# Optimization experiments

Hardware: AMD Instinct MI355X
Metric: run time of the kernel (lower is better)

## Reference

```python
import jax, jax.numpy as jnp
import numpy as np

N_EMBD = 64
N_HEAD = 8
HEAD_SIZE = N_EMBD // N_HEAD  # 8
BLOCK_SIZE = 64
B = 4096
SCALE = N_EMBD ** (-0.5)  # NOTE: source scales by C**-0.5 with C=n_embd, not head_size
EPS = 1e-5


def setup_inputs() -> dict:
    key = jax.random.key(0)
    ks = jax.random.split(key, 12)
    s = 0.02
    return {
        "x": jax.random.normal(ks[0], (B, BLOCK_SIZE, N_EMBD), jnp.float32),
        # per-head q/k/v projections packed as [C, H, hs] (no bias in source)
        "Wq": jax.random.normal(ks[1], (N_EMBD, N_HEAD, HEAD_SIZE), jnp.float32) * s,
        "Wk": jax.random.normal(ks[2], (N_EMBD, N_HEAD, HEAD_SIZE), jnp.float32) * s,
        "Wv": jax.random.normal(ks[3], (N_EMBD, N_HEAD, HEAD_SIZE), jnp.float32) * s,
        "Wo": jax.random.normal(ks[4], (N_EMBD, N_EMBD), jnp.float32) * s,
        "bo": jnp.zeros((N_EMBD,), jnp.float32),
        "W1": jax.random.normal(ks[5], (N_EMBD, 4 * N_EMBD), jnp.float32) * s,
        "b1": jnp.zeros((4 * N_EMBD,), jnp.float32),
        "W2": jax.random.normal(ks[6], (4 * N_EMBD, N_EMBD), jnp.float32) * s,
        "b2": jnp.zeros((N_EMBD,), jnp.float32),
        "g1": jnp.ones((N_EMBD,), jnp.float32),
        "be1": jnp.zeros((N_EMBD,), jnp.float32),
        "g2": jnp.ones((N_EMBD,), jnp.float32),
        "be2": jnp.zeros((N_EMBD,), jnp.float32),
    }


def _layernorm(x, g, b):
    mu = jnp.mean(x, axis=-1, keepdims=True)
    var = jnp.mean(jnp.square(x - mu), axis=-1, keepdims=True)
    return (x - mu) * jax.lax.rsqrt(var + EPS) * g + b


def reference(x, Wq, Wk, Wv, Wo, bo, W1, b1, W2, b2, g1, be1, g2, be2):
    Bb, T, C = x.shape
    # --- multi-head causal self-attention (dropout = identity in eval) ---
    h = _layernorm(x, g1, be1)
    q = jnp.einsum('btc,chd->bhtd', h, Wq)
    k = jnp.einsum('btc,chd->bhtd', h, Wk)
    v = jnp.einsum('btc,chd->bhtd', h, Wv)
    wei = jnp.einsum('bhtd,bhsd->bhts', q, k) * SCALE
    mask = jnp.tril(jnp.ones((T, T), dtype=bool))
    wei = jnp.where(mask, wei, -jnp.inf)
    wei = jax.nn.softmax(wei, axis=-1)
    attn = jnp.einsum('bhts,bhsd->bhtd', wei, v)
    attn = attn.transpose(0, 2, 1, 3).reshape(Bb, T, C)  # concat heads
    x = x + attn @ Wo + bo
    # --- feed-forward ---
    h2 = _layernorm(x, g2, be2)
    ff = jax.nn.relu(h2 @ W1 + b1) @ W2 + b2
    return x + ff
```

## Files before the change

kernel.cpp:

```cpp
#include <hip/hip_runtime.h>
#include <hip/hip_bf16.h>


typedef __attribute__((ext_vector_type(8))) short short8;
typedef __attribute__((ext_vector_type(4))) float f32x4;

#if __has_builtin(__builtin_amdgcn_exp2f)
#define EXP2F(x) __builtin_amdgcn_exp2f(x)
#else
#define EXP2F(x) __expf((x) * 0.69314718056f)
#endif
#if __has_builtin(__builtin_amdgcn_rcpf)
#define RCPF(x) __builtin_amdgcn_rcpf(x)
#else
#define RCPF(x) (1.0f / (x))
#endif

#define ST  72
#define STU 136
#define OH  0
#define OKK 4608
#define OV  9216
#define OP  13896
#define OU  4608
#define NSH 18504

__device__ __forceinline__ short f2bf(float f) {
    unsigned int u = __float_as_uint(f);
    u += 0x7fffu + ((u >> 16) & 1u);
    return (short)(u >> 16);
}
__device__ __forceinline__ unsigned pk2(float a, float b) {
    float2 t; t.x = a; t.y = b;
    __hip_bfloat162 h = __float22bfloat162_rn(t);
    unsigned u; __builtin_memcpy(&u, &h, 4); return u;
}
__device__ __forceinline__ f32x4 mfma16(short8 a, short8 b, f32x4 c) {
    return __builtin_amdgcn_mfma_f32_16x16x32_bf16(a, b, c, 0, 0, 0);
}

__global__ __launch_bounds__(64) void prepack_kernel(
    const float* __restrict__ Wq, const float* __restrict__ Wk,
    const float* __restrict__ Wv, const float* __restrict__ Wo,
    const float* __restrict__ W1, const float* __restrict__ W2,
    short* __restrict__ ws)
{
    int gid = blockIdx.x * 64 + threadIdx.x;
    int lane = gid & 63;
    int fid  = gid >> 6;
    int quad = lane >> 4, nn = lane & 15;
    short8 o;
    if (fid < 24) {
        int tile = fid >> 1, ks = fid & 1;
        const float* Ws = (tile < 4) ? Wq : ((tile < 8) ? Wk : Wv);
        float scale = (tile < 4) ? 0.18033688011f : 1.0f;
        int col = (tile & 3) * 16 + nn;
#pragma unroll
        for (int j = 0; j < 8; ++j)
            o[j] = f2bf(Ws[(ks * 32 + quad * 8 + j) * 64 + col] * scale);
    } else if (fid < 32) {
        int idx = fid - 24, nt = idx >> 1, ks = idx & 1;
#pragma unroll
        for (int j = 0; j < 8; ++j)
            o[j] = f2bf(Wo[(ks * 32 + quad * 8 + j) * 64 + nt * 16 + nn]);
    } else if (fid < 64) {
        int idx = fid - 32, c = idx >> 3, tile = (idx >> 1) & 3, ks = idx & 1;
#pragma unroll
        for (int j = 0; j < 8; ++j)
            o[j] = f2bf(W1[(ks * 32 + quad * 8 + j) * 256 + c * 64 + tile * 16 + nn]);
    } else {
        int idx = fid - 64, c = idx >> 3, nt = (idx >> 1) & 3, ks = idx & 1;
#pragma unroll
        for (int j = 0; j < 8; ++j)
            o[j] = f2bf(W2[(c * 64 + ks * 32 + quad * 8 + j) * 64 + nt * 16 + nn]);
    }
    *(short8*)(ws + (size_t)gid * 8) = o;
}

__global__ __launch_bounds__(256, 4) void block_kernel(
    const float* __restrict__ x,
    const float* __restrict__ bo,
    const float* __restrict__ b1,
    const float* __restrict__ b2,
    const float* __restrict__ g1, const float* __restrict__ be1,
    const float* __restrict__ g2, const float* __restrict__ be2,
    const short8* __restrict__ WB,
    float* __restrict__ out)
{
    __shared__ short sm[NSH];
    const int tid  = threadIdx.x;
    const int wv   = tid >> 6;
    const int lane = tid & 63;
    const int quad = lane >> 4;
    const int nn   = lane & 15;
    const int t_my = wv * 16 + nn;
    const int b    = blockIdx.x;
    const float* xb = x + (size_t)b * 4096;
    const f32x4 zf = {0.f, 0.f, 0.f, 0.f};
    const short8 z8 = {0, 0, 0, 0, 0, 0, 0, 0};

    if (tid < ST) sm[OV + 64 * ST + tid] = (short)0x3F80;
    float xr[16];
    float gv[4], bv[4];
#pragma unroll
    for (int nt = 0; nt < 4; ++nt) { gv[nt] = g1[nt * 16 + nn]; bv[nt] = be1[nt * 16 + nn]; }
#pragma unroll
    for (int nt = 0; nt < 4; ++nt)
#pragma unroll
        for (int r = 0; r < 4; ++r)
            xr[nt * 4 + r] = xb[(wv * 16 + quad * 4 + r) * 64 + nt * 16 + nn];
#pragma unroll
    for (int r = 0; r < 4; ++r) {
        float s1 = 0.f, s2 = 0.f;
#pragma unroll
        for (int nt = 0; nt < 4; ++nt) { float v = xr[nt * 4 + r]; s1 += v; s2 += v * v; }
        s1 += __shfl_xor(s1, 1); s1 += __shfl_xor(s1, 2); s1 += __shfl_xor(s1, 4); s1 += __shfl_xor(s1, 8);
        s2 += __shfl_xor(s2, 1); s2 += __shfl_xor(s2, 2); s2 += __shfl_xor(s2, 4); s2 += __shfl_xor(s2, 8);
        float mu = s1 * 0.015625f;
        float rstd = rsqrtf(s2 * 0.015625f - mu * mu + 1e-5f);
        int base = OH + (wv * 16 + quad * 4 + r) * ST + nn;
#pragma unroll
        for (int nt = 0; nt < 4; ++nt)
            sm[base + nt * 16] = f2bf((xr[nt * 4 + r] - mu) * rstd * gv[nt] + bv[nt]);
    }

    unsigned qp[8];
    {
        short8 hf0 = *(const short8*)&sm[OH + t_my * ST + quad * 8];
        short8 hf1 = *(const short8*)&sm[OH + t_my * ST + 32 + quad * 8];
#pragma unroll
        for (int jt = 0; jt < 4; ++jt) {
            f32x4 a = mfma16(WB[(size_t)(jt * 2 + 0) * 64 + lane], hf0, zf);
            a = mfma16(WB[(size_t)(jt * 2 + 1) * 64 + lane], hf1, a);
            qp[jt * 2 + 0] = pk2(a[0], a[1]);
            qp[jt * 2 + 1] = pk2(a[2], a[3]);
        }
#pragma unroll
        for (int jt = 0; jt < 4; ++jt) {
            f32x4 a = mfma16(WB[(size_t)((4 + jt) * 2 + 0) * 64 + lane], hf0, zf);
            a = mfma16(WB[(size_t)((4 + jt) * 2 + 1) * 64 + lane], hf1, a);
            uint2 w; w.x = pk2(a[0], a[1]); w.y = pk2(a[2], a[3]);
            *(uint2*)&sm[OKK + t_my * ST + jt * 16 + quad * 4] = w;
        }
#pragma unroll
        for (int dt = 0; dt < 4; ++dt) {
            f32x4 a = mfma16(hf0, WB[(size_t)((8 + dt) * 2 + 0) * 64 + lane], zf);
            a = mfma16(hf1, WB[(size_t)((8 + dt) * 2 + 1) * 64 + lane], a);
            uint2 w; w.x = pk2(a[0], a[1]); w.y = pk2(a[2], a[3]);
            *(uint2*)&sm[OV + (dt * 16 + nn) * ST + wv * 16 + quad * 4] = w;
        }
    }
    __syncthreads();

    const bool keep0 = (quad * 4 + 0) <= nn, keep1 = (quad * 4 + 1) <= nn;
    const bool keep2 = (quad * 4 + 2) <= nn, keep3 = (quad * 4 + 3) <= nn;
    const int arow_base = (nn < 8) ? nn : 64;
    const int arow_step = (nn < 8) ? 8 : 0;
    const int nks = (wv < 2) ? 1 : 2;
    const int zhi = nks * 2;
#pragma unroll 1
    for (int h = 0; h < 8; ++h) {
        short8 bq;
        {
            int qsA = ((h & 1) * 2) * 16 + nn, qsB = qsA + 16;
            int qi = (h >> 1) * 2;
            union { unsigned u[4]; short8 s; } bb;
            bb.u[0] = __shfl(qp[qi + 0], qsA);
            bb.u[1] = __shfl(qp[qi + 1], qsA);
            bb.u[2] = __shfl(qp[qi + 0], qsB);
            bb.u[3] = __shfl(qp[qi + 1], qsB);
            bq = bb.s;
        }
        for (int mt = 0; mt <= wv; ++mt) {
            short8 ak = z8;
            if (quad == 0) ak = *(const short8*)&sm[OKK + (mt * 16 + nn) * ST + h * 8];
            f32x4 s = mfma16(ak, bq, zf);
            float e0 = EXP2F(s[0]), e1 = EXP2F(s[1]), e2 = EXP2F(s[2]), e3 = EXP2F(s[3]);
            if (mt == wv) {
                e0 = keep0 ? e0 : 0.f; e1 = keep1 ? e1 : 0.f;
                e2 = keep2 ? e2 : 0.f; e3 = keep3 ? e3 : 0.f;
            }
            uint2 w; w.x = pk2(e0, e1); w.y = pk2(e2, e3);
            *(uint2*)&sm[OP + t_my * ST + mt * 16 + quad * 4] = w;
        }
        for (int mt = wv + 1; mt < zhi; ++mt) {
            uint2 w; w.x = 0u; w.y = 0u;
            *(uint2*)&sm[OP + t_my * ST + mt * 16 + quad * 4] = w;
        }
        const int arow = arow_base + h * arow_step;
        f32x4 pv = zf;
        for (int ks = 0; ks < nks; ++ks) {
            short8 av = *(const short8*)&sm[OV + arow * ST + ks * 32 + quad * 8];
            short8 bp = *(const short8*)&sm[OP + t_my * ST + ks * 32 + quad * 8];
            pv = mfma16(av, bp, pv);
        }
        float denom = __shfl(pv[0], 32 + nn);
        float rd = RCPF(denom);
        if (quad < 2) {
            uint2 w; w.x = pk2(pv[0] * rd, pv[1] * rd); w.y = pk2(pv[2] * rd, pv[3] * rd);
            *(uint2*)&sm[OH + t_my * ST + h * 8 + quad * 4] = w;
        }
    }

    {
        short8 aa0 = *(const short8*)&sm[OH + t_my * ST + quad * 8];
        short8 aa1 = *(const short8*)&sm[OH + t_my * ST + 32 + quad * 8];
#pragma unroll
        for (int nt = 0; nt < 4; ++nt) {
            f32x4 oa = mfma16(aa0, WB[(size_t)(24 + nt * 2 + 0) * 64 + lane], zf);
            oa = mfma16(aa1, WB[(size_t)(24 + nt * 2 + 1) * 64 + lane], oa);
            float bov = bo[nt * 16 + nn];
#pragma unroll
            for (int r = 0; r < 4; ++r) xr[nt * 4 + r] += oa[r] + bov;
        }
    }
#pragma unroll
    for (int nt = 0; nt < 4; ++nt) { gv[nt] = g2[nt * 16 + nn]; bv[nt] = be2[nt * 16 + nn]; }
#pragma unroll
    for (int r = 0; r < 4; ++r) {
        float s1 = 0.f, s2 = 0.f;
#pragma unroll
        for (int nt = 0; nt < 4; ++nt) { float v = xr[nt * 4 + r]; s1 += v; s2 += v * v; }
        s1 += __shfl_xor(s1, 1); s1 += __shfl_xor(s1, 2); s1 += __shfl_xor(s1, 4); s1 += __shfl_xor(s1, 8);
        s2 += __shfl_xor(s2, 1); s2 += __shfl_xor(s2, 2); s2 += __shfl_xor(s2, 4); s2 += __shfl_xor(s2, 8);
        float mu = s1 * 0.015625f;
        float rstd = rsqrtf(s2 * 0.015625f - mu * mu + 1e-5f);
        int base = OP + (wv * 16 + quad * 4 + r) * ST + nn;
#pragma unroll
        for (int nt = 0; nt < 4; ++nt)
            sm[base + nt * 16] = f2bf((xr[nt * 4 + r] - mu) * rstd * gv[nt] + bv[nt]);
    }
    short8 h2f0 = *(const short8*)&sm[OP + t_my * ST + quad * 8];
    short8 h2f1 = *(const short8*)&sm[OP + t_my * ST + 32 + quad * 8];
    __syncthreads();

    f32x4 fa[4];
#pragma unroll
    for (int nt = 0; nt < 4; ++nt) fa[nt] = zf;
#pragma unroll
    for (int c = 0; c < 2; ++c) {
#pragma unroll
        for (int tile = 0; tile < 8; ++tile) {
            int gc = c * 8 + tile;
            int fid = 32 + (gc >> 2) * 8 + (gc & 3) * 2;
            f32x4 u = mfma16(WB[(size_t)fid * 64 + lane], h2f0, zf);
            u = mfma16(WB[(size_t)(fid + 1) * 64 + lane], h2f1, u);
            const float4 bb = *(const float4*)&b1[gc * 16 + quad * 4];
            float u0 = fmaxf(u[0] + bb.x, 0.f), u1 = fmaxf(u[1] + bb.y, 0.f);
            float u2 = fmaxf(u[2] + bb.z, 0.f), u3 = fmaxf(u[3] + bb.w, 0.f);
            uint2 w; w.x = pk2(u0, u1); w.y = pk2(u2, u3);
            *(uint2*)&sm[OU + t_my * STU + tile * 16 + quad * 4] = w;
        }
#pragma unroll
        for (int ks = 0; ks < 4; ++ks) {
            short8 au = *(const short8*)&sm[OU + t_my * STU + ks * 32 + quad * 8];
            int gk = c * 4 + ks;
            int fidb = 64 + (gk >> 1) * 8 + (gk & 1);
#pragma unroll
            for (int nt = 0; nt < 4; ++nt)
                fa[nt] = mfma16(au, WB[(size_t)(fidb + nt * 2) * 64 + lane], fa[nt]);
        }
    }

    float* ob = out + (size_t)b * 4096;
#pragma unroll
    for (int nt = 0; nt < 4; ++nt) {
        float b2v = b2[nt * 16 + nn];
#pragma unroll
        for (int r = 0; r < 4; ++r)
            ob[(wv * 16 + quad * 4 + r) * 64 + nt * 16 + nn] = xr[nt * 4 + r] + fa[nt][r] + b2v;
    }
}

extern "C" void kernel_launch(void* const* d_in, const int* in_sizes, int n_in,
                              void* d_out, int out_size, void* d_ws, size_t ws_size,
                              hipStream_t stream) {
    const float* x   = (const float*)d_in[0];
    const float* Wq  = (const float*)d_in[1];
    const float* Wk  = (const float*)d_in[2];
    const float* Wv  = (const float*)d_in[3];
    const float* Wo  = (const float*)d_in[4];
    const float* bo  = (const float*)d_in[5];
    const float* W1  = (const float*)d_in[6];
    const float* b1  = (const float*)d_in[7];
    const float* W2  = (const float*)d_in[8];
    const float* b2  = (const float*)d_in[9];
    const float* g1  = (const float*)d_in[10];
    const float* be1 = (const float*)d_in[11];
    const float* g2  = (const float*)d_in[12];
    const float* be2 = (const float*)d_in[13];
    short* ws = (short*)d_ws;
    prepack_kernel<<<dim3(96), dim3(64), 0, stream>>>(Wq, Wk, Wv, Wo, W1, W2, ws);
    const int nb = in_sizes[0] / 4096;
    block_kernel<<<dim3(nb), dim3(256), 0, stream>>>(
        x, bo, b1, b2, g1, be1, g2, be2, (const short8*)ws, (float*)d_out);
}
```

Measured before the change: 203.1 us.

## Keep softmax probabilities in registers via shuffles, drop P buffer, raise occupancy

The exponentiated attention scores no longer go through a shared-memory P buffer. They stay in registers and are redistributed into the PV MFMA operand layout with wave shuffles. Dropping the P region shrinks shared memory, and launch bounds go from 4 to 5 blocks per CU. The second layernorm output now reuses the H region. The LN conversions use packed bf16 conversion. The changes trade LDS traffic for many more shuffles and higher register pressure under the tighter occupancy bound.

Measured after the change: 214.7 us. 5.7% more time.

```diff
diff --git a/kernel.cpp b/kernel.cpp
--- a/kernel.cpp
+++ b/kernel.cpp
@@ -21,9 +21,8 @@
 #define OH  0
 #define OKK 4608
 #define OV  9216
-#define OP  13896
 #define OU  4608
-#define NSH 18504
+#define NSH 13896
 
 __device__ __forceinline__ short f2bf(float f) {
     unsigned int u = __float_as_uint(f);
@@ -77,7 +76,36 @@
     *(short8*)(ws + (size_t)gid * 8) = o;
 }
 
-__global__ __launch_bounds__(256, 4) void block_kernel(
+#define QK_TILE(mt, WX, WY)                                                   \
+    {                                                                         \
+        short8 ak = z8;                                                       \
+        if (quad == 0) ak = *(const short8*)&sm[OKK + ((mt) * 16 + nn) * ST + h * 8]; \
+        f32x4 s = mfma16(ak, bq, zf);                                         \
+        float e0 = EXP2F(s[0]), e1 = EXP2F(s[1]);                             \
+        float e2 = EXP2F(s[2]), e3 = EXP2F(s[3]);                             \
+        if ((mt) == wv) {                                                     \
+            e0 = keep0 ? e0 : 0.f; e1 = keep1 ? e1 : 0.f;                     \
+            e2 = keep2 ? e2 : 0.f; e3 = keep3 ? e3 : 0.f;                     \
+        }                                                                     \
+        WX = pk2(e0, e1); WY = pk2(e2, e3);                                   \
+    }
+
+#define PV_KS(ks, WXA, WYA, WXB, WYB)                                         \
+    {                                                                         \
+        unsigned a0 = __shfl(WXA, qa), a1 = __shfl(WXB, qa);                  \
+        unsigned b0 = __shfl(WYA, qa), b1 = __shfl(WYB, qa);                  \
+        unsigned c0 = __shfl(WXA, qb), c1 = __shfl(WXB, qb);                  \
+        unsigned d0 = __shfl(WYA, qb), d1 = __shfl(WYB, qb);                  \
+        union { unsigned u[4]; short8 s; } bb;                                \
+        bb.u[0] = loQ ? a0 : a1;                                              \
+        bb.u[1] = loQ ? b0 : b1;                                              \
+        bb.u[2] = loQ ? c0 : c1;                                              \
+        bb.u[3] = loQ ? d0 : d1;                                              \
+        short8 av = *(const short8*)&sm[OV + arow * ST + (ks) * 32 + quad * 8]; \
+        pv = mfma16(av, bb.s, pv);                                            \
+    }
+
+__global__ __launch_bounds__(256, 5) void block_kernel(
     const float* __restrict__ x,
     const float* __restrict__ bo,
     const float* __restrict__ b1,
@@ -119,9 +147,15 @@
         float mu = s1 * 0.015625f;
         float rstd = rsqrtf(s2 * 0.015625f - mu * mu + 1e-5f);
         int base = OH + (wv * 16 + quad * 4 + r) * ST + nn;
-#pragma unroll
-        for (int nt = 0; nt < 4; ++nt)
-            sm[base + nt * 16] = f2bf((xr[nt * 4 + r] - mu) * rstd * gv[nt] + bv[nt]);
+        float h0 = (xr[0 + r]  - mu) * rstd * gv[0] + bv[0];
+        float h1 = (xr[4 + r]  - mu) * rstd * gv[1] + bv[1];
+        float h2 = (xr[8 + r]  - mu) * rstd * gv[2] + bv[2];
+        float h3 = (xr[12 + r] - mu) * rstd * gv[3] + bv[3];
+        unsigned pA = pk2(h0, h1), pB = pk2(h2, h3);
+        sm[base +  0] = (short)pA;
+        sm[base + 16] = (short)(pA >> 16);
+        sm[base + 32] = (short)pB;
+        sm[base + 48] = (short)(pB >> 16);
     }
 
     unsigned qp[8];
@@ -157,7 +191,9 @@
     const int arow_base = (nn < 8) ? nn : 64;
     const int arow_step = (nn < 8) ? 8 : 0;
     const int nks = (wv < 2) ? 1 : 2;
-    const int zhi = nks * 2;
+    const int qa = (( 2 * quad)      & 3) * 16 + nn;
+    const int qb = ((2 * quad + 1) & 3) * 16 + nn;
+    const bool loQ = (quad < 2);
 #pragma unroll 1
     for (int h = 0; h < 8; ++h) {
         short8 bq;
@@ -171,29 +207,16 @@
             bb.u[3] = __shfl(qp[qi + 1], qsB);
             bq = bb.s;
         }
-        for (int mt = 0; mt <= wv; ++mt) {
-            short8 ak = z8;
-            if (quad == 0) ak = *(const short8*)&sm[OKK + (mt * 16 + nn) * ST + h * 8];
-            f32x4 s = mfma16(ak, bq, zf);
-            float e0 = EXP2F(s[0]), e1 = EXP2F(s[1]), e2 = EXP2F(s[2]), e3 = EXP2F(s[3]);
-            if (mt == wv) {
-                e0 = keep0 ? e0 : 0.f; e1 = keep1 ? e1 : 0.f;
-                e2 = keep2 ? e2 : 0.f; e3 = keep3 ? e3 : 0.f;
-            }
-            uint2 w; w.x = pk2(e0, e1); w.y = pk2(e2, e3);
-            *(uint2*)&sm[OP + t_my * ST + mt * 16 + quad * 4] = w;
-        }
-        for (int mt = wv + 1; mt < zhi; ++mt) {
-            uint2 w; w.x = 0u; w.y = 0u;
-            *(uint2*)&sm[OP + t_my * ST + mt * 16 + quad * 4] = w;
-        }
+        unsigned wx0 = 0, wy0 = 0, wx1 = 0, wy1 = 0;
+        unsigned wx2 = 0, wy2 = 0, wx3 = 0, wy3 = 0;
+        QK_TILE(0, wx0, wy0);
+        if (wv >= 1) QK_TILE(1, wx1, wy1);
+        if (wv >= 2) QK_TILE(2, wx2, wy2);
+        if (wv == 3) QK_TILE(3, wx3, wy3);
         const int arow = arow_base + h * arow_step;
         f32x4 pv = zf;
-        for (int ks = 0; ks < nks; ++ks) {
-            short8 av = *(const short8*)&sm[OV + arow * ST + ks * 32 + quad * 8];
-            short8 bp = *(const short8*)&sm[OP + t_my * ST + ks * 32 + quad * 8];
-            pv = mfma16(av, bp, pv);
-        }
+        PV_KS(0, wx0, wy0, wx1, wy1);
+        if (nks == 2) PV_KS(1, wx2, wy2, wx3, wy3);
         float denom = __shfl(pv[0], 32 + nn);
         float rd = RCPF(denom);
         if (quad < 2) {
@@ -225,13 +248,19 @@
         s2 += __shfl_xor(s2, 1); s2 += __shfl_xor(s2, 2); s2 += __shfl_xor(s2, 4); s2 += __shfl_xor(s2, 8);
         float mu = s1 * 0.015625f;
         float rstd = rsqrtf(s2 * 0.015625f - mu * mu + 1e-5f);
-        int base = OP + (wv * 16 + quad * 4 + r) * ST + nn;
-#pragma unroll
-        for (int nt = 0; nt < 4; ++nt)
-            sm[base + nt * 16] = f2bf((xr[nt * 4 + r] - mu) * rstd * gv[nt] + bv[nt]);
-    }
-    short8 h2f0 = *(const short8*)&sm[OP + t_my * ST + quad * 8];
-    short8 h2f1 = *(const short8*)&sm[OP + t_my * ST + 32 + quad * 8];
+        int base = OH + (wv * 16 + quad * 4 + r) * ST + nn;
+        float h0 = (xr[0 + r]  - mu) * rstd * gv[0] + bv[0];
+        float h1 = (xr[4 + r]  - mu) * rstd * gv[1] + bv[1];
+        float h2 = (xr[8 + r]  - mu) * rstd * gv[2] + bv[2];
+        float h3 = (xr[12 + r] - mu) * rstd * gv[3] + bv[3];
+        unsigned pA = pk2(h0, h1), pB = pk2(h2, h3);
+        sm[base +  0] = (short)pA;
+        sm[base + 16] = (short)(pA >> 16);
+        sm[base + 32] = (short)pB;
+        sm[base + 48] = (short)(pB >> 16);
+    }
+    short8 h2f0 = *(const short8*)&sm[OH + t_my * ST + quad * 8];
+    short8 h2f1 = *(const short8*)&sm[OH + t_my * ST + 32 + quad * 8];
     __syncthreads();
 
     f32x4 fa[4];
```
